# Kernel optimization log

Measured on AMD Instinct MI355X. Metric: run time of the kernel, lower is better.

The kernel has to match this reference:

```python
import jax, jax.numpy as jnp
import numpy as np

N = 50000
E = 800000
IN_DIM = 128
HEADS = 8
OUT_DIM = 32
NEG_SLOPE = 0.2


def setup_inputs() -> dict:
    key = jax.random.key(0)
    k1, k2, k3, k4, k5 = jax.random.split(key, 5)
    x = jax.random.normal(k1, (N, IN_DIM), dtype=jnp.float32)
    edge_index = jax.random.randint(k2, (2, E), 0, N, dtype=jnp.int64)
    batch = jnp.zeros((N,), dtype=jnp.int64)
    # GATConv params: glorot-style scale
    W = jax.random.normal(k3, (IN_DIM, HEADS * OUT_DIM), dtype=jnp.float32) * (1.0 / np.sqrt(IN_DIM))
    att_src = jax.random.normal(k4, (HEADS, OUT_DIM), dtype=jnp.float32) * (1.0 / np.sqrt(OUT_DIM))
    att_dst = jax.random.normal(k5, (HEADS, OUT_DIM), dtype=jnp.float32) * (1.0 / np.sqrt(OUT_DIM))
    bias = jnp.zeros((OUT_DIM,), dtype=jnp.float32)
    return {"x": x, "edge_index": edge_index, "batch": batch,
            "W": W, "att_src": att_src, "att_dst": att_dst, "bias": bias}


def reference(x, edge_index, batch, W, att_src, att_dst, bias):
    n = x.shape[0]
    h = (x @ W).reshape(n, HEADS, OUT_DIM)            # [N, H, C]
    a_src = jnp.einsum('nhc,hc->nh', h, att_src)       # [N, H]
    a_dst = jnp.einsum('nhc,hc->nh', h, att_dst)       # [N, H]
    # add self-loops (PyG default add_self_loops=True)
    loops = jnp.arange(n, dtype=edge_index.dtype)
    src = jnp.concatenate([edge_index[0], loops])
    dst = jnp.concatenate([edge_index[1], loops])
    e = jax.nn.leaky_relu(a_src[src] + a_dst[dst], NEG_SLOPE)  # [E+N, H]
    # scatter-softmax over incoming edges of each dst node
    m = jax.ops.segment_max(e, dst, num_segments=n)    # [N, H]
    m = jax.lax.stop_gradient(m)
    ex = jnp.exp(e - m[dst])
    denom = jax.ops.segment_sum(ex, dst, num_segments=n)
    alpha = ex / denom[dst]                            # [E+N, H]
    msg = h[src] * alpha[..., None]                    # [E+N, H, C]
    out = jax.ops.segment_sum(msg, dst, num_segments=n)  # [N, H, C]
    out = out.mean(axis=1) + bias                      # concat=False -> head mean
    return out
```

## Files before the change

kernel.cpp:

```cpp
#include <hip/hip_runtime.h>
#include <hip/hip_bf16.h>

#define IN_DIM 128
#define HC 256
#define HEADS 8
#define OUT_DIM 32
#define NEG_SLOPE 0.2f
#define ELL_CAP 64

typedef unsigned short ushort_t;
typedef unsigned int uint_t;
typedef __attribute__((ext_vector_type(8))) short bf16x8;
typedef __attribute__((ext_vector_type(8))) unsigned short ushort8_t;
typedef __attribute__((ext_vector_type(4))) float floatx4;

__device__ inline ushort_t f2bf(float f) {
    uint_t u = __float_as_uint(f);
    u = (u + 0x7FFF + ((u >> 16) & 1)) >> 16;
    return (ushort_t)u;
}
__device__ inline float bf2f(ushort_t u) {
    return __uint_as_float(((uint_t)u) << 16);
}
__device__ inline uint_t pkbf(float a, float b) {
    __hip_bfloat162 t = __float22bfloat162_rn(make_float2(a, b));
    union { __hip_bfloat162 h; uint_t u; } c;
    c.h = t;
    return c.u;
}

__global__ __launch_bounds__(256) void prep_build(const float* __restrict__ W,
                                                  ushort_t* __restrict__ Wf,
                                                  const int* __restrict__ esrc,
                                                  const int* __restrict__ edst,
                                                  int* __restrict__ deg,
                                                  ushort_t* __restrict__ ell, int E) {
    const int bid = blockIdx.x;
    const int tid = threadIdx.x;
    if (bid < 16) {
        int t = bid * 256 + tid;
        int lane = t & 63;
        int ks = (t >> 6) & 3;
        int nt = t >> 8;
        int n = nt * 16 + (lane & 15);
        int k0 = ks * 32 + (lane >> 4) * 8;
        float v[8];
#pragma unroll
        for (int j = 0; j < 8; j++) v[j] = W[(size_t)(k0 + j) * HC + n];
        uint4 pk;
        pk.x = pkbf(v[0], v[1]);
        pk.y = pkbf(v[2], v[3]);
        pk.z = pkbf(v[4], v[5]);
        pk.w = pkbf(v[6], v[7]);
        *(uint4*)&Wf[(size_t)t * 8] = pk;
        return;
    }
    int i = (bid - 16) * 256 + tid;
    int base = i * 4;
    if (base + 3 < E) {
        int4 d = *(const int4*)&edst[base];
        int4 s = *(const int4*)&esrc[base];
        int r0 = atomicAdd(&deg[d.x], 1);
        int r1 = atomicAdd(&deg[d.y], 1);
        int r2 = atomicAdd(&deg[d.z], 1);
        int r3 = atomicAdd(&deg[d.w], 1);
        if (r0 < ELL_CAP) ell[d.x * ELL_CAP + r0] = (ushort_t)s.x;
        if (r1 < ELL_CAP) ell[d.y * ELL_CAP + r1] = (ushort_t)s.y;
        if (r2 < ELL_CAP) ell[d.z * ELL_CAP + r2] = (ushort_t)s.z;
        if (r3 < ELL_CAP) ell[d.w * ELL_CAP + r3] = (ushort_t)s.w;
    } else {
        for (int j = base; j < E; j++) {
            int r = atomicAdd(&deg[edst[j]], 1);
            if (r < ELL_CAP) ell[edst[j] * ELL_CAP + r] = (ushort_t)esrc[j];
        }
    }
}

__global__ __launch_bounds__(256) void gemm_mfma(const float* __restrict__ x,
                                                 const ushort_t* __restrict__ Wf,
                                                 const float* __restrict__ att_s,
                                                 const float* __restrict__ att_d,
                                                 ushort_t* __restrict__ h2,
                                                 float* __restrict__ a_src,
                                                 float* __restrict__ a_dst, int N) {
    __shared__ ushort_t xs[128 * 136];
    const int tid = threadIdx.x;
    const int row0 = blockIdx.x * 128;
#pragma unroll
    for (int i = 0; i < 16; i++) {
        int slot = tid + i * 256;
        int r = slot >> 5, kq = slot & 31;
        int gr = row0 + r;
        float4 v = (gr < N) ? *(const float4*)&x[(size_t)gr * IN_DIM + kq * 4]
                            : make_float4(0.f, 0.f, 0.f, 0.f);
        uint2 pk;
        pk.x = pkbf(v.x, v.y);
        pk.y = pkbf(v.z, v.w);
        *(uint2*)&xs[r * 136 + kq * 4] = pk;
    }
    __syncthreads();

    const int lane = tid & 63;
    const int w = tid >> 6;
    const int wrow = (w & 1) * 64;
    const int wcol = (w >> 1) * 64;
    const int m15 = lane & 15, quad = lane >> 4;

#pragma unroll
    for (int ch = 0; ch < 2; ch++) {
        const int colblk = wcol + ch * 128;
        floatx4 acc[4][4] = {};
#pragma unroll
        for (int ks = 0; ks < 4; ks++) {
            bf16x8 xb[4], wa[4];
#pragma unroll
            for (int rt = 0; rt < 4; rt++)
                xb[rt] = *(const bf16x8*)&xs[(wrow + rt * 16 + m15) * 136 + ks * 32 + quad * 8];
#pragma unroll
            for (int ct = 0; ct < 4; ct++) {
                int mtg = (colblk >> 4) + ct;
                wa[ct] = *(const bf16x8*)&Wf[(size_t)(((mtg * 4 + ks) * 64) + lane) * 8];
            }
#pragma unroll
            for (int ct = 0; ct < 4; ct++)
#pragma unroll
                for (int rt = 0; rt < 4; rt++)
                    acc[ct][rt] = __builtin_amdgcn_mfma_f32_16x16x32_bf16(wa[ct], xb[rt], acc[ct][rt], 0, 0, 0);
        }

        const int hb = colblk >> 5;
        float asc[4][4], adc[4][4];
#pragma unroll
        for (int ct = 0; ct < 4; ct++)
#pragma unroll
            for (int reg = 0; reg < 4; reg++) {
                asc[ct][reg] = att_s[colblk + ct * 16 + quad * 4 + reg];
                adc[ct][reg] = att_d[colblk + ct * 16 + quad * 4 + reg];
            }
#pragma unroll
        for (int rt = 0; rt < 4; rt++) {
            int gr = row0 + wrow + rt * 16 + m15;
            bool ok = (gr < N);
            if (ok) {
#pragma unroll
                for (int ct = 0; ct < 4; ct++) {
                    uint2 pk;
                    pk.x = pkbf(acc[ct][rt][0], acc[ct][rt][1]);
                    pk.y = pkbf(acc[ct][rt][2], acc[ct][rt][3]);
                    *(uint2*)&h2[(size_t)gr * HC + colblk + ct * 16 + quad * 4] = pk;
                }
            }
            float sA = 0.f, sB = 0.f, dA = 0.f, dB = 0.f;
#pragma unroll
            for (int reg = 0; reg < 4; reg++) {
                sA += acc[0][rt][reg] * asc[0][reg] + acc[1][rt][reg] * asc[1][reg];
                sB += acc[2][rt][reg] * asc[2][reg] + acc[3][rt][reg] * asc[3][reg];
                dA += acc[0][rt][reg] * adc[0][reg] + acc[1][rt][reg] * adc[1][reg];
                dB += acc[2][rt][reg] * adc[2][reg] + acc[3][rt][reg] * adc[3][reg];
            }
            sA += __shfl_xor(sA, 16, 64); sA += __shfl_xor(sA, 32, 64);
            sB += __shfl_xor(sB, 16, 64); sB += __shfl_xor(sB, 32, 64);
            dA += __shfl_xor(dA, 16, 64); dA += __shfl_xor(dA, 32, 64);
            dB += __shfl_xor(dB, 16, 64); dB += __shfl_xor(dB, 32, 64);
            if (ok && quad == 0) {
                a_src[gr * HEADS + hb]     = sA;
                a_src[gr * HEADS + hb + 1] = sB;
                a_dst[gr * HEADS + hb]     = dA;
                a_dst[gr * HEADS + hb + 1] = dB;
            }
        }
    }
}

__global__ __launch_bounds__(256) void aggregate(const ushort_t* __restrict__ h2,
                                                 const float* __restrict__ a_src,
                                                 const float* __restrict__ a_dst,
                                                 const int* __restrict__ deg,
                                                 const ushort_t* __restrict__ ell,
                                                 const float* __restrict__ bias,
                                                 float* __restrict__ out, int N) {
    int wave = threadIdx.x >> 6;
    int lane = threadIdx.x & 63;
    int n = blockIdx.x * 4 + wave;
    if (n >= N) return;
    int half = lane >> 5;
    int sl = lane & 31;
    int head = sl >> 2;
    int rowoff = sl * 8;

    float adst = a_dst[n * HEADS + head];
    float e = a_src[n * HEADS + head] + adst;
    e = fmaxf(e, NEG_SLOPE * e);
    float p = (half == 0) ? __expf(e) : 0.f;
    ushort8_t hv = *(const ushort8_t*)&h2[(size_t)n * HC + rowoff];
    float acc[8];
#pragma unroll
    for (int j = 0; j < 8; j++) acc[j] = p * bf2f(hv[j]);
    float l = p;

    int dn = __builtin_amdgcn_readfirstlane(deg[n]);
    if (dn > ELL_CAP) dn = ELL_CAP;
    const ushort_t* row = &ell[(size_t)n * ELL_CAP];
    int k = 0;
    for (; k + 7 < dn; k += 8) {
        int sidx[4];
        float ev[4];
        ushort8_t g[4];
#pragma unroll
        for (int j = 0; j < 4; j++) sidx[j] = (int)row[k + 2 * j + half];
#pragma unroll
        for (int j = 0; j < 4; j++) {
            g[j] = *(const ushort8_t*)&h2[(size_t)sidx[j] * HC + rowoff];
            ev[j] = a_src[sidx[j] * HEADS + head];
        }
#pragma unroll
        for (int j = 0; j < 4; j++) {
            float ej = ev[j] + adst;
            ej = fmaxf(ej, NEG_SLOPE * ej);
            float pj = __expf(ej);
#pragma unroll
            for (int c = 0; c < 8; c++) acc[c] += pj * bf2f(g[j][c]);
            l += pj;
        }
    }
    for (; k + 1 < dn; k += 2) {
        int s0 = (int)row[k + half];
        float e0 = a_src[s0 * HEADS + head] + adst;
        ushort8_t g0 = *(const ushort8_t*)&h2[(size_t)s0 * HC + rowoff];
        e0 = fmaxf(e0, NEG_SLOPE * e0);
        float p0 = __expf(e0);
#pragma unroll
        for (int c = 0; c < 8; c++) acc[c] += p0 * bf2f(g0[c]);
        l += p0;
    }
    if (k < dn) {
        int s0 = (int)row[k];
        float e0 = a_src[s0 * HEADS + head] + adst;
        ushort8_t g0 = *(const ushort8_t*)&h2[(size_t)s0 * HC + rowoff];
        e0 = fmaxf(e0, NEG_SLOPE * e0);
        float p0 = (half == 0) ? __expf(e0) : 0.f;
#pragma unroll
        for (int c = 0; c < 8; c++) acc[c] += p0 * bf2f(g0[c]);
        l += p0;
    }

#pragma unroll
    for (int j = 0; j < 8; j++) acc[j] += __shfl_xor(acc[j], 32, 64);
    l += __shfl_xor(l, 32, 64);

    float inv = 0.125f / l;
#pragma unroll
    for (int j = 0; j < 8; j++) acc[j] *= inv;
#pragma unroll
    for (int off = 4; off < 32; off <<= 1)
#pragma unroll
        for (int j = 0; j < 8; j++) acc[j] += __shfl_xor(acc[j], off, 64);

    if (lane < 4) {
        int c8 = sl * 8;
        float4 b0 = *(const float4*)&bias[c8];
        float4 b1 = *(const float4*)&bias[c8 + 4];
        float4 o0 = make_float4(acc[0] + b0.x, acc[1] + b0.y, acc[2] + b0.z, acc[3] + b0.w);
        float4 o1 = make_float4(acc[4] + b1.x, acc[5] + b1.y, acc[6] + b1.z, acc[7] + b1.w);
        *(float4*)&out[(size_t)n * OUT_DIM + c8] = o0;
        *(float4*)&out[(size_t)n * OUT_DIM + c8 + 4] = o1;
    }
}

extern "C" void kernel_launch(void* const* d_in, const int* in_sizes, int n_in,
                              void* d_out, int out_size, void* d_ws, size_t ws_size,
                              hipStream_t stream) {
    const float* x       = (const float*)d_in[0];
    const int*   eidx    = (const int*)d_in[1];
    const float* W       = (const float*)d_in[3];
    const float* att_src = (const float*)d_in[4];
    const float* att_dst = (const float*)d_in[5];
    const float* bias    = (const float*)d_in[6];
    float* out = (float*)d_out;

    const int N = in_sizes[0] / IN_DIM;
    const int E = in_sizes[1] / 2;
    const int* esrc = eidx;
    const int* edst = eidx + E;

    char* wsb = (char*)d_ws;
    size_t off = 0;
    auto alloc = [&](size_t bytes) -> void* {
        void* p = wsb + off;
        off = (off + bytes + 255) & ~(size_t)255;
        return p;
    };
    ushort_t* h2   = (ushort_t*)alloc((size_t)N * HC * 2);
    ushort_t* Wf   = (ushort_t*)alloc((size_t)IN_DIM * HC * 2);
    float*    a_src= (float*)alloc((size_t)N * HEADS * 4);
    float*    a_dst= (float*)alloc((size_t)N * HEADS * 4);
    int*      deg  = (int*)alloc((size_t)N * 4);
    ushort_t* ell  = (ushort_t*)alloc((size_t)N * ELL_CAP * 2);

    const int edge_blocks = (E / 4 + 255) / 256;

    hipMemsetAsync(deg, 0, (size_t)N * 4, stream);
    hipLaunchKernelGGL(prep_build, dim3(16 + edge_blocks), dim3(256), 0, stream,
                       W, Wf, esrc, edst, deg, ell, E);
    hipLaunchKernelGGL(gemm_mfma, dim3((N + 127) / 128), dim3(256), 0, stream,
                       x, Wf, att_src, att_dst, h2, a_src, a_dst, N);
    hipLaunchKernelGGL(aggregate, dim3((N + 3) / 4), dim3(256), 0, stream,
                       h2, a_src, a_dst, deg, ell, bias, out, N);
}
```

Measured before the change: 210.1 us.

## Fuse edge ELL build into GEMM launch and fold deg memset into W prep

Replaces the memset, the W-prep/ELL-build kernel and the GEMM kernel with two launches. A small kernel converts W to bf16 fragments and zeroes the degree array. A second kernel runs the atomic ELL build blocks and the MFMA GEMM blocks side by side in one grid. This removes a launch and a memset and lets the atomic-bound build overlap with the compute-bound GEMM. In exchange, the build blocks carry the GEMM's 34 KB shared-memory allocation, which may lower their occupancy.

```diff
diff --git a/kernel.cpp b/kernel.cpp
--- a/kernel.cpp
+++ b/kernel.cpp
@@ -29,63 +29,67 @@
     return c.u;
 }
 
-__global__ __launch_bounds__(256) void prep_build(const float* __restrict__ W,
-                                                  ushort_t* __restrict__ Wf,
+__global__ __launch_bounds__(256) void prep_w_zero(const float* __restrict__ W,
+                                                   ushort_t* __restrict__ Wf,
+                                                   int* __restrict__ deg, int N) {
+    const int t = blockIdx.x * 256 + threadIdx.x;
+    for (int i = t; i < N; i += 4096) deg[i] = 0;
+
+    int lane = t & 63;
+    int ks = (t >> 6) & 3;
+    int nt = t >> 8;
+    int n = nt * 16 + (lane & 15);
+    int k0 = ks * 32 + (lane >> 4) * 8;
+    float v[8];
+#pragma unroll
+    for (int j = 0; j < 8; j++) v[j] = W[(size_t)(k0 + j) * HC + n];
+    uint4 pk;
+    pk.x = pkbf(v[0], v[1]);
+    pk.y = pkbf(v[2], v[3]);
+    pk.z = pkbf(v[4], v[5]);
+    pk.w = pkbf(v[6], v[7]);
+    *(uint4*)&Wf[(size_t)t * 8] = pk;
+}
+
+__global__ __launch_bounds__(256) void build_gemm(const float* __restrict__ x,
+                                                  const ushort_t* __restrict__ Wf,
+                                                  const float* __restrict__ att_s,
+                                                  const float* __restrict__ att_d,
+                                                  ushort_t* __restrict__ h2,
+                                                  float* __restrict__ a_src,
+                                                  float* __restrict__ a_dst,
                                                   const int* __restrict__ esrc,
                                                   const int* __restrict__ edst,
                                                   int* __restrict__ deg,
-                                                  ushort_t* __restrict__ ell, int E) {
-    const int bid = blockIdx.x;
-    const int tid = threadIdx.x;
-    if (bid < 16) {
-        int t = bid * 256 + tid;
-        int lane = t & 63;
-        int ks = (t >> 6) & 3;
-        int nt = t >> 8;
-        int n = nt * 16 + (lane & 15);
-        int k0 = ks * 32 + (lane >> 4) * 8;
-        float v[8];
-#pragma unroll
-        for (int j = 0; j < 8; j++) v[j] = W[(size_t)(k0 + j) * HC + n];
-        uint4 pk;
-        pk.x = pkbf(v[0], v[1]);
-        pk.y = pkbf(v[2], v[3]);
-        pk.z = pkbf(v[4], v[5]);
-        pk.w = pkbf(v[6], v[7]);
-        *(uint4*)&Wf[(size_t)t * 8] = pk;
-        return;
-    }
-    int i = (bid - 16) * 256 + tid;
-    int base = i * 4;
-    if (base + 3 < E) {
-        int4 d = *(const int4*)&edst[base];
-        int4 s = *(const int4*)&esrc[base];
-        int r0 = atomicAdd(&deg[d.x], 1);
-        int r1 = atomicAdd(&deg[d.y], 1);
-        int r2 = atomicAdd(&deg[d.z], 1);
-        int r3 = atomicAdd(&deg[d.w], 1);
-        if (r0 < ELL_CAP) ell[d.x * ELL_CAP + r0] = (ushort_t)s.x;
-        if (r1 < ELL_CAP) ell[d.y * ELL_CAP + r1] = (ushort_t)s.y;
-        if (r2 < ELL_CAP) ell[d.z * ELL_CAP + r2] = (ushort_t)s.z;
-        if (r3 < ELL_CAP) ell[d.w * ELL_CAP + r3] = (ushort_t)s.w;
-    } else {
-        for (int j = base; j < E; j++) {
-            int r = atomicAdd(&deg[edst[j]], 1);
-            if (r < ELL_CAP) ell[edst[j] * ELL_CAP + r] = (ushort_t)esrc[j];
-        }
-    }
-}
-
-__global__ __launch_bounds__(256) void gemm_mfma(const float* __restrict__ x,
-                                                 const ushort_t* __restrict__ Wf,
-                                                 const float* __restrict__ att_s,
-                                                 const float* __restrict__ att_d,
-                                                 ushort_t* __restrict__ h2,
-                                                 float* __restrict__ a_src,
-                                                 float* __restrict__ a_dst, int N) {
+                                                  ushort_t* __restrict__ ell,
+                                                  int N, int E, int nbuild) {
     __shared__ ushort_t xs[128 * 136];
     const int tid = threadIdx.x;
-    const int row0 = blockIdx.x * 128;
+
+    if ((int)blockIdx.x < nbuild) {
+        int i = blockIdx.x * 256 + tid;
+        int base = i * 4;
+        if (base + 3 < E) {
+            int4 d = *(const int4*)&edst[base];
+            int4 s = *(const int4*)&esrc[base];
+            int r0 = atomicAdd(&deg[d.x], 1);
+            int r1 = atomicAdd(&deg[d.y], 1);
+            int r2 = atomicAdd(&deg[d.z], 1);
+            int r3 = atomicAdd(&deg[d.w], 1);
+            if (r0 < ELL_CAP) ell[d.x * ELL_CAP + r0] = (ushort_t)s.x;
+            if (r1 < ELL_CAP) ell[d.y * ELL_CAP + r1] = (ushort_t)s.y;
+            if (r2 < ELL_CAP) ell[d.z * ELL_CAP + r2] = (ushort_t)s.z;
+            if (r3 < ELL_CAP) ell[d.w * ELL_CAP + r3] = (ushort_t)s.w;
+        } else if (base < E) {
+            for (int j = base; j < E; j++) {
+                int r = atomicAdd(&deg[edst[j]], 1);
+                if (r < ELL_CAP) ell[edst[j] * ELL_CAP + r] = (ushort_t)esrc[j];
+            }
+        }
+        return;
+    }
+
+    const int row0 = ((int)blockIdx.x - nbuild) * 128;
 #pragma unroll
     for (int i = 0; i < 16; i++) {
         int slot = tid + i * 256;
@@ -297,13 +301,13 @@
     int*      deg  = (int*)alloc((size_t)N * 4);
     ushort_t* ell  = (ushort_t*)alloc((size_t)N * ELL_CAP * 2);
 
-    const int edge_blocks = (E / 4 + 255) / 256;
-
-    hipMemsetAsync(deg, 0, (size_t)N * 4, stream);
-    hipLaunchKernelGGL(prep_build, dim3(16 + edge_blocks), dim3(256), 0, stream,
-                       W, Wf, esrc, edst, deg, ell, E);
-    hipLaunchKernelGGL(gemm_mfma, dim3((N + 127) / 128), dim3(256), 0, stream,
-                       x, Wf, att_src, att_dst, h2, a_src, a_dst, N);
+    const int nbuild = (E / 4 + 255) / 256;
+    const int ngemm  = (N + 127) / 128;
+
+    hipLaunchKernelGGL(prep_w_zero, dim3(16), dim3(256), 0, stream, W, Wf, deg, N);
+    hipLaunchKernelGGL(build_gemm, dim3(nbuild + ngemm), dim3(256), 0, stream,
+                       x, Wf, att_src, att_dst, h2, a_src, a_dst,
+                       esrc, edst, deg, ell, N, E, nbuild);
     hipLaunchKernelGGL(aggregate, dim3((N + 3) / 4), dim3(256), 0, stream,
                        h2, a_src, a_dst, deg, ell, bias, out, N);
 }
```

After: 211.7 us. No clear change (+0.8%).

## Fuse prep, GEMM and aggregation into one persistent cooperative kernel

Applied to the files above, without the earlier changes.

Replaces the memset and three kernel launches with a single cooperative persistent kernel separated by grid-wide syncs. The GEMM phase uses 64-row tiles, and the edge-to-ELL build runs after the GEMM through a dynamic atomic work counter. Aggregation then loops over nodes with a grid-stride. The aim is to remove launch gaps and overlap the atomic ELL build's tail with GEMM work, at the cost of grid sync overhead and fewer resident blocks than the original grids.

```diff
diff --git a/kernel.cpp b/kernel.cpp
--- a/kernel.cpp
+++ b/kernel.cpp
@@ -1,5 +1,8 @@
 #include <hip/hip_runtime.h>
 #include <hip/hip_bf16.h>
+#include <hip/hip_cooperative_groups.h>
+
+namespace cg = cooperative_groups;
 
 #define IN_DIM 128
 #define HC 256
@@ -14,11 +17,6 @@
 typedef __attribute__((ext_vector_type(8))) unsigned short ushort8_t;
 typedef __attribute__((ext_vector_type(4))) float floatx4;
 
-__device__ inline ushort_t f2bf(float f) {
-    uint_t u = __float_as_uint(f);
-    u = (u + 0x7FFF + ((u >> 16) & 1)) >> 16;
-    return (ushort_t)u;
-}
 __device__ inline float bf2f(ushort_t u) {
     return __uint_as_float(((uint_t)u) << 16);
 }
@@ -29,97 +27,88 @@
     return c.u;
 }
 
-__global__ __launch_bounds__(256) void prep_build(const float* __restrict__ W,
-                                                  ushort_t* __restrict__ Wf,
-                                                  const int* __restrict__ esrc,
-                                                  const int* __restrict__ edst,
-                                                  int* __restrict__ deg,
-                                                  ushort_t* __restrict__ ell, int E) {
+struct GatParams {
+    const float* x;
+    const float* W;
+    const float* att_s;
+    const float* att_d;
+    const float* bias;
+    const int* esrc;
+    const int* edst;
+    float* out;
+    ushort_t* h2;
+    ushort_t* Wf;
+    float* a_src;
+    float* a_dst;
+    int* deg;
+    ushort_t* ell;
+    int* ctr;
+    int N;
+    int E;
+};
+
+__global__ __launch_bounds__(256) void gat_fused(GatParams p) {
+    __shared__ ushort_t xs[64 * 136];
+    const int tid = threadIdx.x;
     const int bid = blockIdx.x;
-    const int tid = threadIdx.x;
-    if (bid < 16) {
-        int t = bid * 256 + tid;
-        int lane = t & 63;
+    const int nb = gridDim.x;
+    const int gtid = bid * 256 + tid;
+    const int nth = nb * 256;
+    const int lane = tid & 63;
+    const int w = tid >> 6;
+
+    for (int i = gtid; i < p.N; i += nth) p.deg[i] = 0;
+    if (gtid == 0) *p.ctr = 0;
+    if (gtid < 4096) {
+        const int t = gtid;
+        int l = t & 63;
         int ks = (t >> 6) & 3;
-        int nt = t >> 8;
-        int n = nt * 16 + (lane & 15);
-        int k0 = ks * 32 + (lane >> 4) * 8;
+        int nt2 = t >> 8;
+        int n = nt2 * 16 + (l & 15);
+        int k0 = ks * 32 + (l >> 4) * 8;
         float v[8];
 #pragma unroll
-        for (int j = 0; j < 8; j++) v[j] = W[(size_t)(k0 + j) * HC + n];
+        for (int j = 0; j < 8; j++) v[j] = p.W[(size_t)(k0 + j) * HC + n];
         uint4 pk;
         pk.x = pkbf(v[0], v[1]);
         pk.y = pkbf(v[2], v[3]);
         pk.z = pkbf(v[4], v[5]);
         pk.w = pkbf(v[6], v[7]);
-        *(uint4*)&Wf[(size_t)t * 8] = pk;
-        return;
-    }
-    int i = (bid - 16) * 256 + tid;
-    int base = i * 4;
-    if (base + 3 < E) {
-        int4 d = *(const int4*)&edst[base];
-        int4 s = *(const int4*)&esrc[base];
-        int r0 = atomicAdd(&deg[d.x], 1);
-        int r1 = atomicAdd(&deg[d.y], 1);
-        int r2 = atomicAdd(&deg[d.z], 1);
-        int r3 = atomicAdd(&deg[d.w], 1);
-        if (r0 < ELL_CAP) ell[d.x * ELL_CAP + r0] = (ushort_t)s.x;
-        if (r1 < ELL_CAP) ell[d.y * ELL_CAP + r1] = (ushort_t)s.y;
-        if (r2 < ELL_CAP) ell[d.z * ELL_CAP + r2] = (ushort_t)s.z;
-        if (r3 < ELL_CAP) ell[d.w * ELL_CAP + r3] = (ushort_t)s.w;
-    } else {
-        for (int j = base; j < E; j++) {
-            int r = atomicAdd(&deg[edst[j]], 1);
-            if (r < ELL_CAP) ell[edst[j] * ELL_CAP + r] = (ushort_t)esrc[j];
-        }
-    }
-}
-
-__global__ __launch_bounds__(256) void gemm_mfma(const float* __restrict__ x,
-                                                 const ushort_t* __restrict__ Wf,
-                                                 const float* __restrict__ att_s,
-                                                 const float* __restrict__ att_d,
-                                                 ushort_t* __restrict__ h2,
-                                                 float* __restrict__ a_src,
-                                                 float* __restrict__ a_dst, int N) {
-    __shared__ ushort_t xs[128 * 136];
-    const int tid = threadIdx.x;
-    const int row0 = blockIdx.x * 128;
-#pragma unroll
-    for (int i = 0; i < 16; i++) {
-        int slot = tid + i * 256;
-        int r = slot >> 5, kq = slot & 31;
-        int gr = row0 + r;
-        float4 v = (gr < N) ? *(const float4*)&x[(size_t)gr * IN_DIM + kq * 4]
-                            : make_float4(0.f, 0.f, 0.f, 0.f);
-        uint2 pk;
-        pk.x = pkbf(v.x, v.y);
-        pk.y = pkbf(v.z, v.w);
-        *(uint2*)&xs[r * 136 + kq * 4] = pk;
-    }
-    __syncthreads();
-
-    const int lane = tid & 63;
-    const int w = tid >> 6;
-    const int wrow = (w & 1) * 64;
-    const int wcol = (w >> 1) * 64;
+        *(uint4*)&p.Wf[(size_t)t * 8] = pk;
+    }
+    cg::this_grid().sync();
+
+    const int ntiles = (p.N + 63) >> 6;
     const int m15 = lane & 15, quad = lane >> 4;
-
-#pragma unroll
-    for (int ch = 0; ch < 2; ch++) {
-        const int colblk = wcol + ch * 128;
+    const int colblk = w * 64;
+
+    for (int vt = bid; vt < ntiles; vt += nb) {
+        const int row0 = vt * 64;
+#pragma unroll
+        for (int i = 0; i < 8; i++) {
+            int slot = tid + i * 256;
+            int r = slot >> 5, kq = slot & 31;
+            int gr = row0 + r;
+            float4 v = (gr < p.N) ? *(const float4*)&p.x[(size_t)gr * IN_DIM + kq * 4]
+                                  : make_float4(0.f, 0.f, 0.f, 0.f);
+            uint2 pk;
+            pk.x = pkbf(v.x, v.y);
+            pk.y = pkbf(v.z, v.w);
+            *(uint2*)&xs[r * 136 + kq * 4] = pk;
+        }
+        __syncthreads();
+
         floatx4 acc[4][4] = {};
 #pragma unroll
         for (int ks = 0; ks < 4; ks++) {
             bf16x8 xb[4], wa[4];
 #pragma unroll
             for (int rt = 0; rt < 4; rt++)
-                xb[rt] = *(const bf16x8*)&xs[(wrow + rt * 16 + m15) * 136 + ks * 32 + quad * 8];
+                xb[rt] = *(const bf16x8*)&xs[(rt * 16 + m15) * 136 + ks * 32 + quad * 8];
 #pragma unroll
             for (int ct = 0; ct < 4; ct++) {
                 int mtg = (colblk >> 4) + ct;
-                wa[ct] = *(const bf16x8*)&Wf[(size_t)(((mtg * 4 + ks) * 64) + lane) * 8];
+                wa[ct] = *(const bf16x8*)&p.Wf[(size_t)(((mtg * 4 + ks) * 64) + lane) * 8];
             }
 #pragma unroll
             for (int ct = 0; ct < 4; ct++)
@@ -134,20 +123,20 @@
         for (int ct = 0; ct < 4; ct++)
 #pragma unroll
             for (int reg = 0; reg < 4; reg++) {
-                asc[ct][reg] = att_s[colblk + ct * 16 + quad * 4 + reg];
-                adc[ct][reg] = att_d[colblk + ct * 16 + quad * 4 + reg];
+                asc[ct][reg] = p.att_s[colblk + ct * 16 + quad * 4 + reg];
+                adc[ct][reg] = p.att_d[colblk + ct * 16 + quad * 4 + reg];
             }
 #pragma unroll
         for (int rt = 0; rt < 4; rt++) {
-            int gr = row0 + wrow + rt * 16 + m15;
-            bool ok = (gr < N);
+            int gr = row0 + rt * 16 + m15;
+            bool ok = (gr < p.N);
             if (ok) {
 #pragma unroll
                 for (int ct = 0; ct < 4; ct++) {
                     uint2 pk;
                     pk.x = pkbf(acc[ct][rt][0], acc[ct][rt][1]);
                     pk.y = pkbf(acc[ct][rt][2], acc[ct][rt][3]);
-                    *(uint2*)&h2[(size_t)gr * HC + colblk + ct * 16 + quad * 4] = pk;
+                    *(uint2*)&p.h2[(size_t)gr * HC + colblk + ct * 16 + quad * 4] = pk;
                 }
             }
             float sA = 0.f, sB = 0.f, dA = 0.f, dB = 0.f;
@@ -163,107 +152,129 @@
             dA += __shfl_xor(dA, 16, 64); dA += __shfl_xor(dA, 32, 64);
             dB += __shfl_xor(dB, 16, 64); dB += __shfl_xor(dB, 32, 64);
             if (ok && quad == 0) {
-                a_src[gr * HEADS + hb]     = sA;
-                a_src[gr * HEADS + hb + 1] = sB;
-                a_dst[gr * HEADS + hb]     = dA;
-                a_dst[gr * HEADS + hb + 1] = dB;
-            }
-        }
-    }
-}
-
-__global__ __launch_bounds__(256) void aggregate(const ushort_t* __restrict__ h2,
-                                                 const float* __restrict__ a_src,
-                                                 const float* __restrict__ a_dst,
-                                                 const int* __restrict__ deg,
-                                                 const ushort_t* __restrict__ ell,
-                                                 const float* __restrict__ bias,
-                                                 float* __restrict__ out, int N) {
-    int wave = threadIdx.x >> 6;
-    int lane = threadIdx.x & 63;
-    int n = blockIdx.x * 4 + wave;
-    if (n >= N) return;
-    int half = lane >> 5;
-    int sl = lane & 31;
-    int head = sl >> 2;
-    int rowoff = sl * 8;
-
-    float adst = a_dst[n * HEADS + head];
-    float e = a_src[n * HEADS + head] + adst;
-    e = fmaxf(e, NEG_SLOPE * e);
-    float p = (half == 0) ? __expf(e) : 0.f;
-    ushort8_t hv = *(const ushort8_t*)&h2[(size_t)n * HC + rowoff];
-    float acc[8];
-#pragma unroll
-    for (int j = 0; j < 8; j++) acc[j] = p * bf2f(hv[j]);
-    float l = p;
-
-    int dn = __builtin_amdgcn_readfirstlane(deg[n]);
-    if (dn > ELL_CAP) dn = ELL_CAP;
-    const ushort_t* row = &ell[(size_t)n * ELL_CAP];
-    int k = 0;
-    for (; k + 7 < dn; k += 8) {
-        int sidx[4];
-        float ev[4];
-        ushort8_t g[4];
-#pragma unroll
-        for (int j = 0; j < 4; j++) sidx[j] = (int)row[k + 2 * j + half];
-#pragma unroll
-        for (int j = 0; j < 4; j++) {
-            g[j] = *(const ushort8_t*)&h2[(size_t)sidx[j] * HC + rowoff];
-            ev[j] = a_src[sidx[j] * HEADS + head];
-        }
-#pragma unroll
-        for (int j = 0; j < 4; j++) {
-            float ej = ev[j] + adst;
-            ej = fmaxf(ej, NEG_SLOPE * ej);
-            float pj = __expf(ej);
-#pragma unroll
-            for (int c = 0; c < 8; c++) acc[c] += pj * bf2f(g[j][c]);
-            l += pj;
-        }
-    }
-    for (; k + 1 < dn; k += 2) {
-        int s0 = (int)row[k + half];
-        float e0 = a_src[s0 * HEADS + head] + adst;
-        ushort8_t g0 = *(const ushort8_t*)&h2[(size_t)s0 * HC + rowoff];
-        e0 = fmaxf(e0, NEG_SLOPE * e0);
-        float p0 = __expf(e0);
-#pragma unroll
-        for (int c = 0; c < 8; c++) acc[c] += p0 * bf2f(g0[c]);
-        l += p0;
-    }
-    if (k < dn) {
-        int s0 = (int)row[k];
-        float e0 = a_src[s0 * HEADS + head] + adst;
-        ushort8_t g0 = *(const ushort8_t*)&h2[(size_t)s0 * HC + rowoff];
-        e0 = fmaxf(e0, NEG_SLOPE * e0);
-        float p0 = (half == 0) ? __expf(e0) : 0.f;
-#pragma unroll
-        for (int c = 0; c < 8; c++) acc[c] += p0 * bf2f(g0[c]);
-        l += p0;
-    }
-
-#pragma unroll
-    for (int j = 0; j < 8; j++) acc[j] += __shfl_xor(acc[j], 32, 64);
-    l += __shfl_xor(l, 32, 64);
-
-    float inv = 0.125f / l;
-#pragma unroll
-    for (int j = 0; j < 8; j++) acc[j] *= inv;
-#pragma unroll
-    for (int off = 4; off < 32; off <<= 1)
-#pragma unroll
-        for (int j = 0; j < 8; j++) acc[j] += __shfl_xor(acc[j], off, 64);
-
-    if (lane < 4) {
-        int c8 = sl * 8;
-        float4 b0 = *(const float4*)&bias[c8];
-        float4 b1 = *(const float4*)&bias[c8 + 4];
-        float4 o0 = make_float4(acc[0] + b0.x, acc[1] + b0.y, acc[2] + b0.z, acc[3] + b0.w);
-        float4 o1 = make_float4(acc[4] + b1.x, acc[5] + b1.y, acc[6] + b1.z, acc[7] + b1.w);
-        *(float4*)&out[(size_t)n * OUT_DIM + c8] = o0;
-        *(float4*)&out[(size_t)n * OUT_DIM + c8 + 4] = o1;
+                p.a_src[gr * HEADS + hb]     = sA;
+                p.a_src[gr * HEADS + hb + 1] = sB;
+                p.a_dst[gr * HEADS + hb]     = dA;
+                p.a_dst[gr * HEADS + hb + 1] = dB;
+            }
+        }
+        __syncthreads();
+    }
+
+    const int nchunk = (p.E + 3) >> 2;
+    const int nbatch = (nchunk + 63) >> 6;
+    for (;;) {
+        int batch = 0;
+        if (lane == 0) batch = atomicAdd(p.ctr, 1);
+        batch = __shfl(batch, 0, 64);
+        if (batch >= nbatch) break;
+        int c = batch * 64 + lane;
+        if (c < nchunk) {
+            int base = c * 4;
+            if (base + 3 < p.E) {
+                int4 d = *(const int4*)&p.edst[base];
+                int4 s = *(const int4*)&p.esrc[base];
+                int r0 = atomicAdd(&p.deg[d.x], 1);
+                int r1 = atomicAdd(&p.deg[d.y], 1);
+                int r2 = atomicAdd(&p.deg[d.z], 1);
+                int r3 = atomicAdd(&p.deg[d.w], 1);
+                if (r0 < ELL_CAP) p.ell[d.x * ELL_CAP + r0] = (ushort_t)s.x;
+                if (r1 < ELL_CAP) p.ell[d.y * ELL_CAP + r1] = (ushort_t)s.y;
+                if (r2 < ELL_CAP) p.ell[d.z * ELL_CAP + r2] = (ushort_t)s.z;
+                if (r3 < ELL_CAP) p.ell[d.w * ELL_CAP + r3] = (ushort_t)s.w;
+            } else {
+                for (int j = base; j < p.E; j++) {
+                    int r = atomicAdd(&p.deg[p.edst[j]], 1);
+                    if (r < ELL_CAP) p.ell[p.edst[j] * ELL_CAP + r] = (ushort_t)p.esrc[j];
+                }
+            }
+        }
+    }
+    cg::this_grid().sync();
+
+    const int half = lane >> 5;
+    const int sl = lane & 31;
+    const int head = sl >> 2;
+    const int rowoff = sl * 8;
+    const int nwv = nb * 4;
+    for (int n = bid * 4 + w; n < p.N; n += nwv) {
+        float adst = p.a_dst[n * HEADS + head];
+        float e = p.a_src[n * HEADS + head] + adst;
+        e = fmaxf(e, NEG_SLOPE * e);
+        float pp = (half == 0) ? __expf(e) : 0.f;
+        ushort8_t hv = *(const ushort8_t*)&p.h2[(size_t)n * HC + rowoff];
+        float acc[8];
+#pragma unroll
+        for (int j = 0; j < 8; j++) acc[j] = pp * bf2f(hv[j]);
+        float l = pp;
+
+        int dn = __builtin_amdgcn_readfirstlane(p.deg[n]);
+        if (dn > ELL_CAP) dn = ELL_CAP;
+        const ushort_t* row = &p.ell[(size_t)n * ELL_CAP];
+        int k = 0;
+        for (; k + 7 < dn; k += 8) {
+            int sidx[4];
+            float ev[4];
+            ushort8_t g[4];
+#pragma unroll
+            for (int j = 0; j < 4; j++) sidx[j] = (int)row[k + 2 * j + half];
+#pragma unroll
+            for (int j = 0; j < 4; j++) {
+                g[j] = *(const ushort8_t*)&p.h2[(size_t)sidx[j] * HC + rowoff];
+                ev[j] = p.a_src[sidx[j] * HEADS + head];
+            }
+#pragma unroll
+            for (int j = 0; j < 4; j++) {
+                float ej = ev[j] + adst;
+                ej = fmaxf(ej, NEG_SLOPE * ej);
+                float pj = __expf(ej);
+#pragma unroll
+                for (int c = 0; c < 8; c++) acc[c] += pj * bf2f(g[j][c]);
+                l += pj;
+            }
+        }
+        for (; k + 1 < dn; k += 2) {
+            int s0 = (int)row[k + half];
+            float e0 = p.a_src[s0 * HEADS + head] + adst;
+            ushort8_t g0 = *(const ushort8_t*)&p.h2[(size_t)s0 * HC + rowoff];
+            e0 = fmaxf(e0, NEG_SLOPE * e0);
+            float p0 = __expf(e0);
+#pragma unroll
+            for (int c = 0; c < 8; c++) acc[c] += p0 * bf2f(g0[c]);
+            l += p0;
+        }
+        if (k < dn) {
+            int s0 = (int)row[k];
+            float e0 = p.a_src[s0 * HEADS + head] + adst;
+            ushort8_t g0 = *(const ushort8_t*)&p.h2[(size_t)s0 * HC + rowoff];
+            e0 = fmaxf(e0, NEG_SLOPE * e0);
+            float p0 = (half == 0) ? __expf(e0) : 0.f;
+#pragma unroll
+            for (int c = 0; c < 8; c++) acc[c] += p0 * bf2f(g0[c]);
+            l += p0;
+        }
+
+#pragma unroll
+        for (int j = 0; j < 8; j++) acc[j] += __shfl_xor(acc[j], 32, 64);
+        l += __shfl_xor(l, 32, 64);
+
+        float inv = 0.125f / l;
+#pragma unroll
+        for (int j = 0; j < 8; j++) acc[j] *= inv;
+#pragma unroll
+        for (int off = 4; off < 32; off <<= 1)
+#pragma unroll
+            for (int j = 0; j < 8; j++) acc[j] += __shfl_xor(acc[j], off, 64);
+
+        if (lane < 4) {
+            int c8 = sl * 8;
+            float4 b0 = *(const float4*)&p.bias[c8];
+            float4 b1 = *(const float4*)&p.bias[c8 + 4];
+            float4 o0 = make_float4(acc[0] + b0.x, acc[1] + b0.y, acc[2] + b0.z, acc[3] + b0.w);
+            float4 o1 = make_float4(acc[4] + b1.x, acc[5] + b1.y, acc[6] + b1.z, acc[7] + b1.w);
+            *(float4*)&p.out[(size_t)n * OUT_DIM + c8] = o0;
+            *(float4*)&p.out[(size_t)n * OUT_DIM + c8 + 4] = o1;
+        }
     }
 }
 
@@ -296,14 +307,29 @@
     float*    a_dst= (float*)alloc((size_t)N * HEADS * 4);
     int*      deg  = (int*)alloc((size_t)N * 4);
     ushort_t* ell  = (ushort_t*)alloc((size_t)N * ELL_CAP * 2);
-
-    const int edge_blocks = (E / 4 + 255) / 256;
-
-    hipMemsetAsync(deg, 0, (size_t)N * 4, stream);
-    hipLaunchKernelGGL(prep_build, dim3(16 + edge_blocks), dim3(256), 0, stream,
-                       W, Wf, esrc, edst, deg, ell, E);
-    hipLaunchKernelGGL(gemm_mfma, dim3((N + 127) / 128), dim3(256), 0, stream,
-                       x, Wf, att_src, att_dst, h2, a_src, a_dst, N);
-    hipLaunchKernelGGL(aggregate, dim3((N + 3) / 4), dim3(256), 0, stream,
-                       h2, a_src, a_dst, deg, ell, bias, out, N);
+    int*      ctr  = (int*)alloc(256);
+
+    GatParams hp;
+    hp.x = x; hp.W = W; hp.att_s = att_src; hp.att_d = att_dst; hp.bias = bias;
+    hp.esrc = esrc; hp.edst = edst; hp.out = out;
+    hp.h2 = h2; hp.Wf = Wf; hp.a_src = a_src; hp.a_dst = a_dst;
+    hp.deg = deg; hp.ell = ell; hp.ctr = ctr;
+    hp.N = N; hp.E = E;
+
+    static int gridBlocks = 0;
+    if (gridBlocks == 0) {
+        int maxB = 0;
+        if (hipOccupancyMaxActiveBlocksPerMultiprocessor(&maxB, gat_fused, 256, 0) != hipSuccess || maxB < 1)
+            maxB = 4;
+        int dev = 0;
+        hipGetDevice(&dev);
+        int cus = 0;
+        if (hipDeviceGetAttribute(&cus, hipDeviceAttributeMultiprocessorCount, dev) != hipSuccess || cus < 1)
+            cus = 256;
+        gridBlocks = maxB * cus;
+        if (gridBlocks > 4096) gridBlocks = 4096;
+    }
+
+    void* args[] = { (void*)&hp };
+    hipLaunchCooperativeKernel(gat_fused, dim3(gridBlocks), dim3(256), args, 0, stream);
 }
```

Measured after the change: 388.2 us. 1.85x slower.

## Split aggregation per head across blocks with transposed ELL and atomic output

Applied to the files above, without the earlier changes.

The aggregation kernel now launches eight times as many blocks, each handling one head for four nodes. Each wave gathers eight edges at a time, with 8 lanes covering the head's 32 channels, and head results are combined through float atomicAdd into an output zeroed in the prep kernel. The ELL adjacency and the attention logits are stored transposed (slot-major and head-major) so the per-head loads coalesce across nodes. The aim is more parallelism and fewer wasted lanes per edge, at the cost of output atomics, the extra zeroing pass, redundant index loads for each head, and scattered atomic writes during ELL construction.

```diff
diff --git a/kernel.cpp b/kernel.cpp
--- a/kernel.cpp
+++ b/kernel.cpp
@@ -11,14 +11,8 @@
 typedef unsigned short ushort_t;
 typedef unsigned int uint_t;
 typedef __attribute__((ext_vector_type(8))) short bf16x8;
-typedef __attribute__((ext_vector_type(8))) unsigned short ushort8_t;
 typedef __attribute__((ext_vector_type(4))) float floatx4;
 
-__device__ inline ushort_t f2bf(float f) {
-    uint_t u = __float_as_uint(f);
-    u = (u + 0x7FFF + ((u >> 16) & 1)) >> 16;
-    return (ushort_t)u;
-}
 __device__ inline float bf2f(ushort_t u) {
     return __uint_as_float(((uint_t)u) << 16);
 }
@@ -34,11 +28,16 @@
                                                   const int* __restrict__ esrc,
                                                   const int* __restrict__ edst,
                                                   int* __restrict__ deg,
-                                                  ushort_t* __restrict__ ell, int E) {
+                                                  ushort_t* __restrict__ ellT,
+                                                  float* __restrict__ out,
+                                                  int N, int E) {
     const int bid = blockIdx.x;
     const int tid = threadIdx.x;
     if (bid < 16) {
         int t = bid * 256 + tid;
+        float4 z4 = make_float4(0.f, 0.f, 0.f, 0.f);
+        for (int i = t; i < N * 8; i += 4096) ((float4*)out)[i] = z4;
+
         int lane = t & 63;
         int ks = (t >> 6) & 3;
         int nt = t >> 8;
@@ -64,14 +63,14 @@
         int r1 = atomicAdd(&deg[d.y], 1);
         int r2 = atomicAdd(&deg[d.z], 1);
         int r3 = atomicAdd(&deg[d.w], 1);
-        if (r0 < ELL_CAP) ell[d.x * ELL_CAP + r0] = (ushort_t)s.x;
-        if (r1 < ELL_CAP) ell[d.y * ELL_CAP + r1] = (ushort_t)s.y;
-        if (r2 < ELL_CAP) ell[d.z * ELL_CAP + r2] = (ushort_t)s.z;
-        if (r3 < ELL_CAP) ell[d.w * ELL_CAP + r3] = (ushort_t)s.w;
+        if (r0 < ELL_CAP) ellT[(size_t)r0 * N + d.x] = (ushort_t)s.x;
+        if (r1 < ELL_CAP) ellT[(size_t)r1 * N + d.y] = (ushort_t)s.y;
+        if (r2 < ELL_CAP) ellT[(size_t)r2 * N + d.z] = (ushort_t)s.z;
+        if (r3 < ELL_CAP) ellT[(size_t)r3 * N + d.w] = (ushort_t)s.w;
     } else {
         for (int j = base; j < E; j++) {
             int r = atomicAdd(&deg[edst[j]], 1);
-            if (r < ELL_CAP) ell[edst[j] * ELL_CAP + r] = (ushort_t)esrc[j];
+            if (r < ELL_CAP) ellT[(size_t)r * N + edst[j]] = (ushort_t)esrc[j];
         }
     }
 }
@@ -81,8 +80,8 @@
                                                  const float* __restrict__ att_s,
                                                  const float* __restrict__ att_d,
                                                  ushort_t* __restrict__ h2,
-                                                 float* __restrict__ a_src,
-                                                 float* __restrict__ a_dst, int N) {
+                                                 float* __restrict__ a_srcT,
+                                                 float* __restrict__ a_dstT, int N) {
     __shared__ ushort_t xs[128 * 136];
     const int tid = threadIdx.x;
     const int row0 = blockIdx.x * 128;
@@ -163,107 +162,98 @@
             dA += __shfl_xor(dA, 16, 64); dA += __shfl_xor(dA, 32, 64);
             dB += __shfl_xor(dB, 16, 64); dB += __shfl_xor(dB, 32, 64);
             if (ok && quad == 0) {
-                a_src[gr * HEADS + hb]     = sA;
-                a_src[gr * HEADS + hb + 1] = sB;
-                a_dst[gr * HEADS + hb]     = dA;
-                a_dst[gr * HEADS + hb + 1] = dB;
+                a_srcT[(size_t)hb * N + gr]       = sA;
+                a_srcT[(size_t)(hb + 1) * N + gr] = sB;
+                a_dstT[(size_t)hb * N + gr]       = dA;
+                a_dstT[(size_t)(hb + 1) * N + gr] = dB;
             }
         }
     }
 }
 
 __global__ __launch_bounds__(256) void aggregate(const ushort_t* __restrict__ h2,
-                                                 const float* __restrict__ a_src,
-                                                 const float* __restrict__ a_dst,
+                                                 const float* __restrict__ a_srcT,
+                                                 const float* __restrict__ a_dstT,
                                                  const int* __restrict__ deg,
-                                                 const ushort_t* __restrict__ ell,
+                                                 const ushort_t* __restrict__ ellT,
                                                  const float* __restrict__ bias,
                                                  float* __restrict__ out, int N) {
-    int wave = threadIdx.x >> 6;
-    int lane = threadIdx.x & 63;
-    int n = blockIdx.x * 4 + wave;
+    const int wave = threadIdx.x >> 6;
+    const int lane = threadIdx.x & 63;
+    const int seg = blockIdx.x & 7;
+    const int chunk = blockIdx.x >> 3;
+    const int n = chunk * 4 + wave;
     if (n >= N) return;
-    int half = lane >> 5;
-    int sl = lane & 31;
-    int head = sl >> 2;
-    int rowoff = sl * 8;
-
-    float adst = a_dst[n * HEADS + head];
-    float e = a_src[n * HEADS + head] + adst;
-    e = fmaxf(e, NEG_SLOPE * e);
-    float p = (half == 0) ? __expf(e) : 0.f;
-    ushort8_t hv = *(const ushort8_t*)&h2[(size_t)n * HC + rowoff];
-    float acc[8];
-#pragma unroll
-    for (int j = 0; j < 8; j++) acc[j] = p * bf2f(hv[j]);
-    float l = p;
-
-    int dn = __builtin_amdgcn_readfirstlane(deg[n]);
+
+    const int slot = lane >> 3;
+    const int pos = lane & 7;
+    const int coff = seg * 32 + pos * 4;
+    const float* asg = &a_srcT[(size_t)seg * N];
+
+    const float adst = a_dstT[(size_t)seg * N + n];
+
+    float acc[4] = {0.f, 0.f, 0.f, 0.f};
+    float l = 0.f;
+
+    {
+        float e = asg[n] + adst;
+        e = fmaxf(e, NEG_SLOPE * e);
+        float p = (slot == 0) ? __expf(e) : 0.f;
+        uint2 g = *(const uint2*)&h2[(size_t)n * HC + coff];
+        acc[0] += p * bf2f((ushort_t)(g.x & 0xffff));
+        acc[1] += p * bf2f((ushort_t)(g.x >> 16));
+        acc[2] += p * bf2f((ushort_t)(g.y & 0xffff));
+        acc[3] += p * bf2f((ushort_t)(g.y >> 16));
+        l += p;
+    }
+
+    int dn = deg[n];
     if (dn > ELL_CAP) dn = ELL_CAP;
-    const ushort_t* row = &ell[(size_t)n * ELL_CAP];
-    int k = 0;
-    for (; k + 7 < dn; k += 8) {
-        int sidx[4];
-        float ev[4];
-        ushort8_t g[4];
-#pragma unroll
-        for (int j = 0; j < 4; j++) sidx[j] = (int)row[k + 2 * j + half];
-#pragma unroll
-        for (int j = 0; j < 4; j++) {
-            g[j] = *(const ushort8_t*)&h2[(size_t)sidx[j] * HC + rowoff];
-            ev[j] = a_src[sidx[j] * HEADS + head];
-        }
-#pragma unroll
-        for (int j = 0; j < 4; j++) {
-            float ej = ev[j] + adst;
-            ej = fmaxf(ej, NEG_SLOPE * ej);
-            float pj = __expf(ej);
-#pragma unroll
-            for (int c = 0; c < 8; c++) acc[c] += pj * bf2f(g[j][c]);
-            l += pj;
-        }
-    }
-    for (; k + 1 < dn; k += 2) {
-        int s0 = (int)row[k + half];
-        float e0 = a_src[s0 * HEADS + head] + adst;
-        ushort8_t g0 = *(const ushort8_t*)&h2[(size_t)s0 * HC + rowoff];
-        e0 = fmaxf(e0, NEG_SLOPE * e0);
-        float p0 = __expf(e0);
-#pragma unroll
-        for (int c = 0; c < 8; c++) acc[c] += p0 * bf2f(g0[c]);
-        l += p0;
-    }
-    if (k < dn) {
-        int s0 = (int)row[k];
-        float e0 = a_src[s0 * HEADS + head] + adst;
-        ushort8_t g0 = *(const ushort8_t*)&h2[(size_t)s0 * HC + rowoff];
-        e0 = fmaxf(e0, NEG_SLOPE * e0);
-        float p0 = (half == 0) ? __expf(e0) : 0.f;
-#pragma unroll
-        for (int c = 0; c < 8; c++) acc[c] += p0 * bf2f(g0[c]);
-        l += p0;
-    }
-
-#pragma unroll
-    for (int j = 0; j < 8; j++) acc[j] += __shfl_xor(acc[j], 32, 64);
-    l += __shfl_xor(l, 32, 64);
-
-    float inv = 0.125f / l;
-#pragma unroll
-    for (int j = 0; j < 8; j++) acc[j] *= inv;
-#pragma unroll
-    for (int off = 4; off < 32; off <<= 1)
-#pragma unroll
-        for (int j = 0; j < 8; j++) acc[j] += __shfl_xor(acc[j], off, 64);
-
-    if (lane < 4) {
-        int c8 = sl * 8;
-        float4 b0 = *(const float4*)&bias[c8];
-        float4 b1 = *(const float4*)&bias[c8 + 4];
-        float4 o0 = make_float4(acc[0] + b0.x, acc[1] + b0.y, acc[2] + b0.z, acc[3] + b0.w);
-        float4 o1 = make_float4(acc[4] + b1.x, acc[5] + b1.y, acc[6] + b1.z, acc[7] + b1.w);
-        *(float4*)&out[(size_t)n * OUT_DIM + c8] = o0;
-        *(float4*)&out[(size_t)n * OUT_DIM + c8 + 4] = o1;
+
+    for (int kb = 0; kb < dn; kb += 24) {
+        int si[3];
+        float ev[3];
+        uint2 g[3];
+        bool m[3];
+#pragma unroll
+        for (int j = 0; j < 3; j++) {
+            int k = kb + slot + j * 8;
+            m[j] = (k < dn);
+            int ks = m[j] ? k : 0;
+            si[j] = (int)ellT[(size_t)ks * N + n];
+        }
+#pragma unroll
+        for (int j = 0; j < 3; j++) ev[j] = asg[si[j]];
+#pragma unroll
+        for (int j = 0; j < 3; j++) g[j] = *(const uint2*)&h2[(size_t)si[j] * HC + coff];
+#pragma unroll
+        for (int j = 0; j < 3; j++) {
+            float e = ev[j] + adst;
+            e = fmaxf(e, NEG_SLOPE * e);
+            float p = m[j] ? __expf(e) : 0.f;
+            acc[0] += p * bf2f((ushort_t)(g[j].x & 0xffff));
+            acc[1] += p * bf2f((ushort_t)(g[j].x >> 16));
+            acc[2] += p * bf2f((ushort_t)(g[j].y & 0xffff));
+            acc[3] += p * bf2f((ushort_t)(g[j].y >> 16));
+            l += p;
+        }
+    }
+
+#pragma unroll
+    for (int off = 8; off < 64; off <<= 1) {
+#pragma unroll
+        for (int j = 0; j < 4; j++) acc[j] += __shfl_xor(acc[j], off, 64);
+        l += __shfl_xor(l, off, 64);
+    }
+
+    if (slot == 0) {
+        float inv = 0.125f / l;
+#pragma unroll
+        for (int c = 0; c < 4; c++) {
+            float v = acc[c] * inv;
+            if (seg == 0) v += bias[pos * 4 + c];
+            atomicAdd(&out[(size_t)n * OUT_DIM + pos * 4 + c], v);
+        }
     }
 }
 
@@ -290,20 +280,20 @@
         off = (off + bytes + 255) & ~(size_t)255;
         return p;
     };
-    ushort_t* h2   = (ushort_t*)alloc((size_t)N * HC * 2);
-    ushort_t* Wf   = (ushort_t*)alloc((size_t)IN_DIM * HC * 2);
-    float*    a_src= (float*)alloc((size_t)N * HEADS * 4);
-    float*    a_dst= (float*)alloc((size_t)N * HEADS * 4);
-    int*      deg  = (int*)alloc((size_t)N * 4);
-    ushort_t* ell  = (ushort_t*)alloc((size_t)N * ELL_CAP * 2);
+    ushort_t* h2    = (ushort_t*)alloc((size_t)N * HC * 2);
+    ushort_t* Wf    = (ushort_t*)alloc((size_t)IN_DIM * HC * 2);
+    float*    a_srcT= (float*)alloc((size_t)N * HEADS * 4);
+    float*    a_dstT= (float*)alloc((size_t)N * HEADS * 4);
+    int*      deg   = (int*)alloc((size_t)N * 4);
+    ushort_t* ellT  = (ushort_t*)alloc((size_t)N * ELL_CAP * 2);
 
     const int edge_blocks = (E / 4 + 255) / 256;
 
     hipMemsetAsync(deg, 0, (size_t)N * 4, stream);
     hipLaunchKernelGGL(prep_build, dim3(16 + edge_blocks), dim3(256), 0, stream,
-                       W, Wf, esrc, edst, deg, ell, E);
+                       W, Wf, esrc, edst, deg, ellT, out, N, E);
     hipLaunchKernelGGL(gemm_mfma, dim3((N + 127) / 128), dim3(256), 0, stream,
-                       x, Wf, att_src, att_dst, h2, a_src, a_dst, N);
-    hipLaunchKernelGGL(aggregate, dim3((N + 3) / 4), dim3(256), 0, stream,
-                       h2, a_src, a_dst, deg, ell, bias, out, N);
-}
+                       x, Wf, att_src, att_dst, h2, a_srcT, a_dstT, N);
+    hipLaunchKernelGGL(aggregate, dim3(((N + 3) / 4) * 8), dim3(256), 0, stream,
+                       h2, a_srcT, a_dstT, deg, ellT, bias, out, N);
+}
```

New measurement: 361.0 us. 1.72x slower.
